# Kernel optimization log

Measured on AMD Instinct MI355X. Metric: run time of the kernel, lower is better.

## Reference

```python
import math
import jax, jax.numpy as jnp
import numpy as np

SM_K = 5

def make_sm_kernel(kernel_size=SM_K, sigma_e=1.2, sigma_i=1.4):
    center = kernel_size // 2
    xx, yy = jnp.meshgrid(jnp.arange(kernel_size, dtype=jnp.float32),
                          jnp.arange(kernel_size, dtype=jnp.float32), indexing='ij')
    xx = xx - center
    yy = yy - center
    g_e = jnp.exp(-(xx ** 2 + yy ** 2) / (2.0 * sigma_e ** 2))
    g_i = jnp.exp(-(xx ** 2 + yy ** 2) / (2.0 * sigma_i ** 2))
    dog = g_e / (2.0 * math.pi * sigma_e ** 2) - g_i / (2.0 * math.pi * sigma_i ** 2)
    return dog / dog[center, center]  # (5,5), normalized so center == 1


def setup_inputs() -> dict:
    key = jax.random.key(0)
    k1, k2 = jax.random.split(key)
    B, Cin, H, W = 16, 64, 128, 128
    Cout, K = 64, 5
    x = jax.random.normal(k1, (B, Cin, H, W), dtype=jnp.float32)
    weight_range = 25.0 / math.sqrt(Cin * K * K)
    weight = weight_range * jnp.abs(jax.random.normal(k2, (Cout, Cin, K, K), dtype=jnp.float32))
    return {"x": x, "weight": weight}


def reference(x, weight):
    PAD = 2
    dn = ('NCHW', 'OIHW', 'NCHW')
    Cout = weight.shape[0]
    K = weight.shape[-1]

    # symmetric_pad -> F.pad reflect
    xp = jnp.pad(x, ((0, 0), (0, 0), (PAD, PAD), (PAD, PAD)), mode='reflect')

    # w = weight.abs(); F.normalize(w, p=2, dim=1): L2 norm over in_channels per (o, kh, kw)
    w = jnp.abs(weight)
    nrm = jnp.sqrt(jnp.sum(w * w, axis=1, keepdims=True))
    w_n = w / jnp.maximum(nrm, 1e-12)

    # cosine similarity: conv with normalized weights / input patch norm
    conv = jax.lax.conv_general_dilated(xp, w_n, (1, 1), 'VALID', dimension_numbers=dn)
    # conv(x^2, ones_like(w)) yields identical values for every output channel;
    # compute once with a single-output-channel ones kernel and broadcast.
    ones_k = jnp.ones((1, x.shape[1], K, K), dtype=x.dtype)
    xsq_sum = jax.lax.conv_general_dilated(xp * xp, ones_k, (1, 1), 'VALID', dimension_numbers=dn)
    y = conv / jnp.sqrt(xsq_sum + 1e-8)  # (B, Cout, H, W)

    # surround modulation: depthwise conv with fixed 5x5 DoG kernel, padding 2
    sm = make_sm_kernel()
    sm_k = jnp.broadcast_to(sm[None, None].astype(y.dtype), (Cout, 1, SM_K, SM_K))
    y = jax.lax.conv_general_dilated(y, sm_k, (1, 1), [(SM_K // 2, SM_K // 2)] * 2,
                                     dimension_numbers=dn, feature_group_count=Cout)
    return y
```

## Files before the change

kernel.cpp:

```cpp
#include <hip/hip_runtime.h>
#include <hip/hip_bf16.h>
#include <math.h>

#define B_   16
#define CIN  64
#define COUT 64
#define H_   128
#define W_   128
#define KK   25
#define HW   (H_ * W_)

typedef short  bf16x8 __attribute__((ext_vector_type(8)));
typedef short  s16x4  __attribute__((ext_vector_type(4)));
typedef float  f32x16 __attribute__((ext_vector_type(16)));
typedef float  f32x4  __attribute__((ext_vector_type(4)));
typedef float  f32x2  __attribute__((ext_vector_type(2)));

__device__ __forceinline__ short f2bs(float v) {
    __hip_bfloat16 h = __float2bfloat16(v);
    return *reinterpret_cast<short*>(&h);
}
__device__ __forceinline__ float bs2f(short s) {
    unsigned int u = ((unsigned int)(unsigned short)s) << 16;
    return __uint_as_float(u);
}

__global__ __launch_bounds__(256) void k_wprep(const float* __restrict__ w,
                                               short* __restrict__ wnb2) {
    __shared__ float wl[CIN * KK];
    __shared__ float inv[KK];
    const int o   = blockIdx.x;
    const int tid = threadIdx.x;

    for (int idx = tid; idx < CIN * KK; idx += 256)
        wl[idx] = w[(size_t)o * (CIN * KK) + idx];
    __syncthreads();
    if (tid < KK) {
        float s = 0.f;
        #pragma unroll 8
        for (int i = 0; i < CIN; ++i) { float v = wl[i * KK + tid]; s += v * v; }
        inv[tid] = 1.f / fmaxf(sqrtf(s), 1e-12f);
    }
    __syncthreads();
    const int tt = o >> 5, n = o & 31;
    for (int idx = tid; idx < CIN * KK; idx += 256) {
        int ci = idx & 63, kk = idx >> 6;
        int ks = ci >> 4, q = (ci >> 3) & 1, j = ci & 7;
        int l = q * 32 + n;
        wnb2[((size_t)((kk * 4 + ks) * 2 + tt) * 64 + l) * 8 + j] =
            f2bs(fabsf(wl[ci * KK + kk]) * inv[kk]);
    }
}

#define XP 40
#define NR 12
#define NC 36
#define NS (NR * NC)
#define TP 264

__global__ __launch_bounds__(256) void k_conv(const float* __restrict__ x,
                                              const short* __restrict__ wnb2,
                                              __hip_bfloat16* __restrict__ t) {
    __shared__ short xin[NS * XP];
    __shared__ float s2win[NS];
    __shared__ int   soff[NS];
    __shared__ float xsq[256];

    const int tid  = threadIdx.x;
    const int lane = tid & 63;
    const int wv   = tid >> 6;
    const int n    = lane & 31;
    const int q    = lane >> 5;
    const int b    = blockIdx.z;
    const int h0   = blockIdx.y * 8;
    const int w0   = blockIdx.x * 32;

    for (int s = tid; s < NS; s += 256) {
        int r = s / NC, c = s - r * NC;
        int hh = h0 - 2 + r; hh = hh < 0 ? -hh : (hh > H_ - 1 ? 2 * (H_ - 1) - hh : hh);
        int ww = w0 - 2 + c; ww = ww < 0 ? -ww : (ww > W_ - 1 ? 2 * (W_ - 1) - ww : ww);
        soff[s] = hh * W_ + ww;
    }
    __syncthreads();

    const float* xb = x + (size_t)b * CIN * HW;
    const short* wb = wnb2 + (size_t)lane * 8;

    f32x16 acc00, acc01, acc10, acc11;
    #pragma unroll
    for (int i = 0; i < 16; ++i) { acc00[i] = 0.f; acc01[i] = 0.f; acc10[i] = 0.f; acc11[i] = 0.f; }

    #pragma unroll
    for (int half = 0; half < 2; ++half) {
        const float* xh = xb + (size_t)(half * 32) * HW;
        for (int idx = tid; idx < NS * 32; idx += 256) {
            int s  = idx % NS;
            int ci = idx / NS;
            xin[s * XP + ci] = f2bs(xh[(size_t)ci * HW + soff[s]]);
        }
        __syncthreads();

        for (int s = tid; s < NS; s += 256) {
            const bf16x8* p = (const bf16x8*)&xin[s * XP];
            float a = (half == 0) ? 0.f : s2win[s];
            #pragma unroll
            for (int c8 = 0; c8 < 4; ++c8) {
                bf16x8 v = p[c8];
                #pragma unroll
                for (int j = 0; j < 8; ++j) { float f = bs2f(v[j]); a += f * f; }
            }
            s2win[s] = a;
        }

        #pragma unroll 5
        for (int kk = 0; kk < KK; ++kk) {
            const int kh = kk / 5, kw = kk % 5;
            const int sp0 = (2 * wv + kh) * NC + n + kw;
            #pragma unroll
            for (int ks2 = 0; ks2 < 2; ++ks2) {
                const int ks = half * 2 + ks2;
                const int ko = ks2 * 16 + q * 8;
                bf16x8 a0 = *(const bf16x8*)&xin[sp0 * XP + ko];
                bf16x8 a1 = *(const bf16x8*)&xin[(sp0 + NC) * XP + ko];
                bf16x8 b0 = *(const bf16x8*)&wb[(size_t)((kk * 4 + ks) * 2 + 0) * 512];
                bf16x8 b1 = *(const bf16x8*)&wb[(size_t)((kk * 4 + ks) * 2 + 1) * 512];
                acc00 = __builtin_amdgcn_mfma_f32_32x32x16_bf16(a0, b0, acc00, 0, 0, 0);
                acc01 = __builtin_amdgcn_mfma_f32_32x32x16_bf16(a0, b1, acc01, 0, 0, 0);
                acc10 = __builtin_amdgcn_mfma_f32_32x32x16_bf16(a1, b0, acc10, 0, 0, 0);
                acc11 = __builtin_amdgcn_mfma_f32_32x32x16_bf16(a1, b1, acc11, 0, 0, 0);
            }
        }
        __syncthreads();
    }

    {
        int hr = tid >> 5, cl = tid & 31;
        float a = 0.f;
        #pragma unroll
        for (int kh = 0; kh < 5; ++kh)
            #pragma unroll
            for (int kw = 0; kw < 5; ++kw)
                a += s2win[(hr + kh) * NC + cl + kw];
        xsq[tid] = a;
    }
    __syncthreads();

    short* trans = xin;
    const int hrA = 2 * wv, hrB = 2 * wv + 1;
    #pragma unroll
    for (int g4 = 0; g4 < 4; ++g4) {
        int wc0 = 8 * g4 + 4 * q;
        s16x4 v00, v01, v10, v11;
        #pragma unroll
        for (int j = 0; j < 4; ++j) {
            float ia = rsqrtf(xsq[hrA * 32 + wc0 + j] + 1e-8f);
            float ib = rsqrtf(xsq[hrB * 32 + wc0 + j] + 1e-8f);
            v00[j] = f2bs(acc00[4 * g4 + j] * ia);
            v01[j] = f2bs(acc01[4 * g4 + j] * ia);
            v10[j] = f2bs(acc10[4 * g4 + j] * ib);
            v11[j] = f2bs(acc11[4 * g4 + j] * ib);
        }
        *(s16x4*)&trans[n * TP        + hrA * 32 + wc0] = v00;
        *(s16x4*)&trans[(32 + n) * TP + hrA * 32 + wc0] = v01;
        *(s16x4*)&trans[n * TP        + hrB * 32 + wc0] = v10;
        *(s16x4*)&trans[(32 + n) * TP + hrB * 32 + wc0] = v11;
    }
    __syncthreads();

    #pragma unroll
    for (int u = tid; u < 512; u += 256) {
        int oc = u >> 3, hr = u & 7;
        const short* src = &trans[oc * TP + hr * 32];
        __hip_bfloat16* dst = t + ((size_t)(b * COUT + oc) * H_ + h0 + hr) * W_ + w0;
        float4 a0 = *(const float4*)(src);
        float4 a1 = *(const float4*)(src + 8);
        float4 a2 = *(const float4*)(src + 16);
        float4 a3 = *(const float4*)(src + 24);
        *(float4*)(dst)      = a0;
        *(float4*)(dst + 8)  = a1;
        *(float4*)(dst + 16) = a2;
        *(float4*)(dst + 24) = a3;
    }
}

__global__ __launch_bounds__(256) void k_dog(const __hip_bfloat16* __restrict__ t,
                                             float* __restrict__ out) {
    __shared__ float tile[36 * 136];
    __shared__ float sm_s[25];
    const int bo  = blockIdx.y;
    const int h0  = blockIdx.x * 32;
    const int tid = threadIdx.x;

    if (tid < 25) {
        const float se2 = 2.f * 1.2f * 1.2f;
        const float si2 = 2.f * 1.4f * 1.4f;
        const float twopi = 6.28318530717958647692f;
        const float ae = 1.f / (twopi * 1.2f * 1.2f);
        const float ai = 1.f / (twopi * 1.4f * 1.4f);
        const float c0 = ae - ai;
        int dx = tid / 5 - 2, dy = tid % 5 - 2;
        float r2 = (float)(dx * dx + dy * dy);
        sm_s[tid] = (ae * expf(-r2 / se2) - ai * expf(-r2 / si2)) / c0;
    }

    const __hip_bfloat16* tc = t + (size_t)bo * HW;
    for (int idx = tid; idx < 36 * 16; idx += 256) {
        int rr = idx >> 4, g = idx & 15;
        int hh = h0 - 2 + rr;
        float v[8];
        if (hh >= 0 && hh < H_) {
            bf16x8 a = *(const bf16x8*)&tc[hh * W_ + g * 8];
            #pragma unroll
            for (int j = 0; j < 8; ++j) v[j] = bs2f(a[j]);
        } else {
            #pragma unroll
            for (int j = 0; j < 8; ++j) v[j] = 0.f;
        }
        float* dst = &tile[rr * 136 + 2 + g * 8];
        *(f32x2*)(dst)     = (f32x2){v[0], v[1]};
        *(f32x4*)(dst + 2) = (f32x4){v[2], v[3], v[4], v[5]};
        *(f32x2*)(dst + 6) = (f32x2){v[6], v[7]};
    }
    if (tid < 36 * 4) {
        int rr = tid >> 2, c = tid & 3;
        tile[rr * 136 + (c < 2 ? c : 128 + c)] = 0.f;
    }
    __syncthreads();

    float smr[25];
    #pragma unroll
    for (int kk = 0; kk < 25; ++kk) smr[kk] = sm_s[kk];

    const int cq = tid & 31;
    const int r0 = tid >> 5;
    #pragma unroll
    for (int rr = 0; rr < 4; ++rr) {
        int r = r0 + 8 * rr;
        float s0 = 0.f, s1 = 0.f, s2 = 0.f, s3 = 0.f;
        #pragma unroll
        for (int kh = 0; kh < 5; ++kh) {
            const float* row = &tile[(r + kh) * 136 + cq * 4];
            f32x4 v0 = *(const f32x4*)(row);
            f32x4 v1 = *(const f32x4*)(row + 4);
            float vv[8] = { v0[0], v0[1], v0[2], v0[3], v1[0], v1[1], v1[2], v1[3] };
            #pragma unroll
            for (int kw = 0; kw < 5; ++kw) {
                float cf = smr[kh * 5 + kw];
                s0 += cf * vv[kw];
                s1 += cf * vv[kw + 1];
                s2 += cf * vv[kw + 2];
                s3 += cf * vv[kw + 3];
            }
        }
        float4 o4 = make_float4(s0, s1, s2, s3);
        *(float4*)&out[((size_t)bo * H_ + h0 + r) * W_ + cq * 4] = o4;
    }
}

extern "C" void kernel_launch(void* const* d_in, const int* in_sizes, int n_in,
                              void* d_out, int out_size, void* d_ws, size_t ws_size,
                              hipStream_t stream) {
    const float* x = (const float*)d_in[0];
    const float* w = (const float*)d_in[1];

    __hip_bfloat16* t = (__hip_bfloat16*)d_ws;

    short* wnb2 = (short*)((char*)d_out + (size_t)67108864 - 204800);

    k_wprep<<<COUT, 256, 0, stream>>>(w, wnb2);

    dim3 g2(W_ / 32, H_ / 8, B_);
    k_conv<<<g2, 256, 0, stream>>>(x, wnb2, t);

    dim3 g3(H_ / 32, B_ * COUT);
    k_dog<<<g3, 256, 0, stream>>>(t, (float*)d_out);
}
```

Measured before the change: 225.7 us.

## Precompute channel-last bf16 input and per-pixel squared sums in a prep kernel

Adds a k_xprep kernel that transposes x from NCHW fp32 into two channel-last bf16 planes of 32 channels each, and writes per-pixel sums of x^2 over all channels. k_conv then fills its shared-memory halo with 16-byte vector copies instead of strided scalar fp32 gathers with per-element conversion. It also reads the precomputed squared sums rather than recomputing them from shared memory. In exchange it adds a full extra pass over the input plus scratch writes placed in the output buffer. The squared sums are now taken from the fp32 values instead of the bf16-rounded ones.

```diff
diff --git a/kernel.cpp b/kernel.cpp
--- a/kernel.cpp
+++ b/kernel.cpp
@@ -9,6 +9,7 @@
 #define W_   128
 #define KK   25
 #define HW   (H_ * W_)
+#define XT_PLANE ((size_t)B_ * HW * 32)
 
 typedef short  bf16x8 __attribute__((ext_vector_type(8)));
 typedef short  s16x4  __attribute__((ext_vector_type(4)));
@@ -52,13 +53,55 @@
     }
 }
 
+__global__ __launch_bounds__(256) void k_xprep(const float* __restrict__ x,
+                                               short* __restrict__ xt,
+                                               float* __restrict__ xsqg) {
+    __shared__ float tile[64][65];
+    __shared__ float ps[4][64];
+    const int b = blockIdx.z, h = blockIdx.y, w0 = blockIdx.x * 64;
+    const int tid = threadIdx.x;
+
+    const float* xb = x + (size_t)b * CIN * HW + h * W_ + w0;
+    {
+        int wl = tid & 63, c0 = tid >> 6;
+        float sq = 0.f;
+        #pragma unroll
+        for (int cc = 0; cc < 16; ++cc) {
+            float v = xb[(size_t)(c0 * 16 + cc) * HW + wl];
+            tile[c0 * 16 + cc][wl] = v;
+            sq += v * v;
+        }
+        ps[c0][wl] = sq;
+    }
+    __syncthreads();
+
+    const size_t pixbase = (size_t)b * HW + h * W_ + w0;
+    if (tid < 64)
+        xsqg[pixbase + tid] = ps[0][tid] + ps[1][tid] + ps[2][tid] + ps[3][tid];
+
+    {
+        int c8 = tid & 7;
+        int half = c8 >> 2, sl = c8 & 3;
+        short* dp = xt + (size_t)half * XT_PLANE;
+        #pragma unroll
+        for (int rep = 0; rep < 2; ++rep) {
+            int p = (tid >> 3) + rep * 32;
+            bf16x8 v;
+            #pragma unroll
+            for (int j = 0; j < 8; ++j) v[j] = f2bs(tile[c8 * 8 + j][p]);
+            *(bf16x8*)&dp[(pixbase + p) * 32 + sl * 8] = v;
+        }
+    }
+}
+
 #define XP 40
 #define NR 12
 #define NC 36
 #define NS (NR * NC)
 #define TP 264
 
-__global__ __launch_bounds__(256) void k_conv(const float* __restrict__ x,
+__global__ __launch_bounds__(256) void k_conv(const short* __restrict__ xt,
+                                              const float* __restrict__ xsqg,
                                               const short* __restrict__ wnb2,
                                               __hip_bfloat16* __restrict__ t) {
     __shared__ short xin[NS * XP];
@@ -75,15 +118,29 @@
     const int h0   = blockIdx.y * 8;
     const int w0   = blockIdx.x * 32;
 
+    const size_t pixbase = (size_t)b * HW;
+
     for (int s = tid; s < NS; s += 256) {
         int r = s / NC, c = s - r * NC;
         int hh = h0 - 2 + r; hh = hh < 0 ? -hh : (hh > H_ - 1 ? 2 * (H_ - 1) - hh : hh);
         int ww = w0 - 2 + c; ww = ww < 0 ? -ww : (ww > W_ - 1 ? 2 * (W_ - 1) - ww : ww);
-        soff[s] = hh * W_ + ww;
-    }
-    __syncthreads();
-
-    const float* xb = x + (size_t)b * CIN * HW;
+        int off = hh * W_ + ww;
+        soff[s] = off;
+        s2win[s] = xsqg[pixbase + off];
+    }
+    __syncthreads();
+
+    {
+        int hr = tid >> 5, cl = tid & 31;
+        float a = 0.f;
+        #pragma unroll
+        for (int kh = 0; kh < 5; ++kh)
+            #pragma unroll
+            for (int kw = 0; kw < 5; ++kw)
+                a += s2win[(hr + kh) * NC + cl + kw];
+        xsq[tid] = a;
+    }
+
     const short* wb = wnb2 + (size_t)lane * 8;
 
     f32x16 acc00, acc01, acc10, acc11;
@@ -92,25 +149,13 @@
 
     #pragma unroll
     for (int half = 0; half < 2; ++half) {
-        const float* xh = xb + (size_t)(half * 32) * HW;
-        for (int idx = tid; idx < NS * 32; idx += 256) {
-            int s  = idx % NS;
-            int ci = idx / NS;
-            xin[s * XP + ci] = f2bs(xh[(size_t)ci * HW + soff[s]]);
+        const short* xph = xt + (size_t)half * XT_PLANE + pixbase * 32;
+        for (int i = tid; i < NS * 4; i += 256) {
+            int s = i >> 2, c8 = i & 3;
+            *(bf16x8*)&xin[s * XP + c8 * 8] =
+                *(const bf16x8*)&xph[(size_t)soff[s] * 32 + c8 * 8];
         }
         __syncthreads();
-
-        for (int s = tid; s < NS; s += 256) {
-            const bf16x8* p = (const bf16x8*)&xin[s * XP];
-            float a = (half == 0) ? 0.f : s2win[s];
-            #pragma unroll
-            for (int c8 = 0; c8 < 4; ++c8) {
-                bf16x8 v = p[c8];
-                #pragma unroll
-                for (int j = 0; j < 8; ++j) { float f = bs2f(v[j]); a += f * f; }
-            }
-            s2win[s] = a;
-        }
 
         #pragma unroll 5
         for (int kk = 0; kk < KK; ++kk) {
@@ -133,18 +178,6 @@
         __syncthreads();
     }
 
-    {
-        int hr = tid >> 5, cl = tid & 31;
-        float a = 0.f;
-        #pragma unroll
-        for (int kh = 0; kh < 5; ++kh)
-            #pragma unroll
-            for (int kw = 0; kw < 5; ++kw)
-                a += s2win[(hr + kh) * NC + cl + kw];
-        xsq[tid] = a;
-    }
-    __syncthreads();
-
     short* trans = xin;
     const int hrA = 2 * wv, hrB = 2 * wv + 1;
     #pragma unroll
@@ -265,12 +298,17 @@
 
     __hip_bfloat16* t = (__hip_bfloat16*)d_ws;
 
-    short* wnb2 = (short*)((char*)d_out + (size_t)67108864 - 204800);
+    short* xt    = (short*)d_out;
+    float* xsqg  = (float*)((char*)d_out + 33554432);
+    short* wnb2  = (short*)((char*)d_out + (size_t)67108864 - 204800);
 
     k_wprep<<<COUT, 256, 0, stream>>>(w, wnb2);
 
+    dim3 gx(W_ / 64, H_, B_);
+    k_xprep<<<gx, 256, 0, stream>>>(x, xt, xsqg);
+
     dim3 g2(W_ / 32, H_ / 8, B_);
-    k_conv<<<g2, 256, 0, stream>>>(x, wnb2, t);
+    k_conv<<<g2, 256, 0, stream>>>(xt, xsqg, wnb2, t);
 
     dim3 g3(H_ / 32, B_ * COUT);
     k_dog<<<g3, 256, 0, stream>>>(t, (float*)d_out);
```

Result: faster. 215.2 us (-4.7%).
